# Optimization experiments

Measured on AMD Instinct MI355X. Metric: run time of the kernel, lower is better.

Reference implementation:

```python
import jax, jax.numpy as jnp
import numpy as np

HIDDEN = [256, 256, 256]
COND = 30
NB_STEPS = 20  # Clenshaw-Curtis quadrature order -> NB_STEPS+1 nodes


def cc_weights_steps(nb_steps):
    # Clenshaw-Curtis weights/nodes on [-1, 1] (UMNN compute_cc_weights)
    lam = np.arange(nb_steps + 1, dtype=np.float64).reshape(-1, 1)
    lam = np.cos(lam @ lam.T * np.pi / nb_steps)
    lam[:, 0] *= 0.5
    lam[:, -1] *= 0.5
    lam = lam * 2.0 / nb_steps
    W = np.arange(nb_steps + 1, dtype=np.float64).reshape(-1, 1)
    W[1::2] = 0.0
    W = 2.0 / (1.0 - W ** 2)
    W[0] = 1.0
    W[1::2] = 0.0
    cc_w = (lam.T @ W).flatten()          # [S]
    steps = np.cos(np.arange(nb_steps + 1) * np.pi / nb_steps)  # [S]
    return jnp.asarray(cc_w, jnp.float32), jnp.asarray(steps, jnp.float32)


def mlp(inp, Ws, bs):
    # IntegrandNet: Linear+ReLU chain, final layer ELU(x)+1 (strictly positive)
    y = inp
    n = len(Ws)
    for i in range(n):
        y = y @ Ws[i] + bs[i]
        y = jax.nn.relu(y) if i < n - 1 else jax.nn.elu(y) + 1.0
    return y[..., 0]


def setup_inputs() -> dict:
    key = jax.random.key(0)
    ks = jax.random.split(key, 12)
    B, D = 512, 32
    x = jax.random.normal(ks[0], (B, D), jnp.float32)
    h = jax.random.normal(ks[1], (B, D, COND), jnp.float32)
    dims = [1 + COND] + HIDDEN + [1]
    params = {}
    for i in range(len(dims) - 1):
        params[f"W{i}"] = jax.random.normal(ks[2 + 2 * i], (dims[i], dims[i + 1]), jnp.float32) / np.sqrt(dims[i]).astype(np.float32)
        params[f"b{i}"] = jnp.zeros((dims[i + 1],), jnp.float32)
    return {"x": x, "h": h, **params}


def reference(x, h, W0, b0, W1, b1, W2, b2, W3, b3):
    Ws = [W0, W1, W2, W3]
    bs = [b0, b1, b2, b3]
    B, D = x.shape
    S = NB_STEPS + 1
    cc_w, steps = cc_weights_steps(NB_STEPS)
    # x0 = 0, xT = x -> quadrature nodes X = xT * (steps + 1) / 2, shape [B, S, D]
    X = x[:, None, :] * (steps[None, :, None] + 1.0) * 0.5
    hb = jnp.broadcast_to(h[:, None, :, :], (B, S, D, COND))
    inp = jnp.concatenate([X[..., None], hb], axis=-1)  # [B, S, D, 1+COND]
    f = mlp(inp, Ws, bs)                                 # [B, S, D] positive integrand
    z_est = jnp.einsum('bsd,s->bd', f, cc_w) * x * 0.5   # integral over [0, x]
    z = z_est + h[:, :, 0]                               # add offset z0
    # second output: integrand evaluated at x (the transform's Jacobian diag)
    inp_x = jnp.concatenate([x[..., None], h], axis=-1)  # [B, D, 1+COND]
    jac = mlp(inp_x, Ws, bs)                             # [B, D]
    return z, jac
```

## Files before the change

### kernel.cpp

```cpp
#include <hip/hip_runtime.h>
#include <math.h>

#define NB        512
#define ND        32
#define NCOND     30
#define NS        21
#define NBD       (NB*ND)
#define NROWS     (NBD*NS)
#define MBLK      64
#define NBLOCKS   (NROWS/MBLK)

#define W0P_ELEMS (1*16*64*8)
#define W1P_ELEMS (8*16*64*8)
#define W3P_ELEMS (8*64*8)
#define WP_TOTAL  (W0P_ELEMS + 2*W1P_ELEMS + W3P_ELEMS)

typedef __bf16 bf8 __attribute__((ext_vector_type(8)));
typedef float  fx4 __attribute__((ext_vector_type(4)));
typedef unsigned short us8 __attribute__((ext_vector_type(8)));

__device__ __forceinline__ unsigned short f2bf(float f) {
  unsigned int u = __float_as_uint(f);
  u += 0x7FFFu + ((u >> 16) & 1u);
  return (unsigned short)(u >> 16);
}

__global__ void prep_pack(const float* __restrict__ W0,
                          const float* __restrict__ W1,
                          const float* __restrict__ W2,
                          const float* __restrict__ W3,
                          unsigned short* __restrict__ wp) {
  int t = blockIdx.x * blockDim.x + threadIdx.x;
  if (t >= WP_TOTAL / 8) return;
  int base = t * 8;
  us8 out;
  if (base >= W0P_ELEMS + 2 * W1P_ELEMS) {
    int rem  = base - (W0P_ELEMS + 2 * W1P_ELEMS);
    int lane = (rem >> 3) & 63;
    int ktl  = rem >> 9;
    int k0   = ktl * 32 + (lane >> 4) * 8;
#pragma unroll
    for (int i = 0; i < 8; ++i)
      out[i] = ((lane & 15) == 0) ? f2bf(W3[k0 + i]) : (unsigned short)0;
  } else {
    const float* W; int rem, K;
    if (base < W0P_ELEMS)                  { W = W0; rem = base;                 K = 31;  }
    else if (base < W0P_ELEMS + W1P_ELEMS) { W = W1; rem = base - W0P_ELEMS;     K = 256; }
    else                                   { W = W2; rem = base - W0P_ELEMS - W1P_ELEMS; K = 256; }
    int lane = (rem >> 3) & 63;
    int ct   = (rem >> 9) & 15;
    int ktl  =  rem >> 13;
    int j  = ct * 16 + (lane & 15);
    int k0 = ktl * 32 + (lane >> 4) * 8;
#pragma unroll
    for (int i = 0; i < 8; ++i) {
      int k = k0 + i;
      out[i] = (k < K) ? f2bf(W[k * 256 + j]) : (unsigned short)0;
    }
  }
  *reinterpret_cast<us8*>(wp + base) = out;
}


#define ACC_BIAS(BIAS)                                                           \
  {                                                                              \
    float4 bq0 = *reinterpret_cast<const float4*>((BIAS) + (cgrp * 4 + 0) * 16 + khalf * 4); \
    float4 bq1 = *reinterpret_cast<const float4*>((BIAS) + (cgrp * 4 + 1) * 16 + khalf * 4); \
    float4 bq2 = *reinterpret_cast<const float4*>((BIAS) + (cgrp * 4 + 2) * 16 + khalf * 4); \
    float4 bq3 = *reinterpret_cast<const float4*>((BIAS) + (cgrp * 4 + 3) * 16 + khalf * 4); \
    _Pragma("unroll")                                                            \
    for (int rt = 0; rt < 4; ++rt) {                                             \
      acc[rt][0] = fx4{bq0.x, bq0.y, bq0.z, bq0.w};                              \
      acc[rt][1] = fx4{bq1.x, bq1.y, bq1.z, bq1.w};                              \
      acc[rt][2] = fx4{bq2.x, bq2.y, bq2.z, bq2.w};                              \
      acc[rt][3] = fx4{bq3.x, bq3.y, bq3.z, bq3.w};                              \
    }                                                                            \
  }

#define LOADW4(S0,S1,S2,S3, WB, KT)                                              \
  S0 = *reinterpret_cast<const bf8*>((WB) + (((KT) * 16 + cgrp * 4 + 0) * 64 + lane) * 8); \
  S1 = *reinterpret_cast<const bf8*>((WB) + (((KT) * 16 + cgrp * 4 + 1) * 64 + lane) * 8); \
  S2 = *reinterpret_cast<const bf8*>((WB) + (((KT) * 16 + cgrp * 4 + 2) * 64 + lane) * 8); \
  S3 = *reinterpret_cast<const bf8*>((WB) + (((KT) * 16 + cgrp * 4 + 3) * 64 + lane) * 8);

#define AOFF(M, KT) (((unsigned)((M) * 512 + (KT) * 64 + khalf * 16)) ^ ((unsigned)(((M) & 15) << 4)))

#define KSTEP(SRC, W0_,W1_,W2_,W3_, KT)                                          \
  {                                                                              \
    bf8 a0 = *reinterpret_cast<const bf8*>((SRC) + AOFF( 0 + colb, KT));         \
    bf8 a1 = *reinterpret_cast<const bf8*>((SRC) + AOFF(16 + colb, KT));         \
    bf8 a2 = *reinterpret_cast<const bf8*>((SRC) + AOFF(32 + colb, KT));         \
    bf8 a3 = *reinterpret_cast<const bf8*>((SRC) + AOFF(48 + colb, KT));         \
    __builtin_amdgcn_s_setprio(1);                                               \
    acc[0][0] = __builtin_amdgcn_mfma_f32_16x16x32_bf16(W0_, a0, acc[0][0], 0, 0, 0); \
    acc[0][1] = __builtin_amdgcn_mfma_f32_16x16x32_bf16(W1_, a0, acc[0][1], 0, 0, 0); \
    acc[0][2] = __builtin_amdgcn_mfma_f32_16x16x32_bf16(W2_, a0, acc[0][2], 0, 0, 0); \
    acc[0][3] = __builtin_amdgcn_mfma_f32_16x16x32_bf16(W3_, a0, acc[0][3], 0, 0, 0); \
    acc[1][0] = __builtin_amdgcn_mfma_f32_16x16x32_bf16(W0_, a1, acc[1][0], 0, 0, 0); \
    acc[1][1] = __builtin_amdgcn_mfma_f32_16x16x32_bf16(W1_, a1, acc[1][1], 0, 0, 0); \
    acc[1][2] = __builtin_amdgcn_mfma_f32_16x16x32_bf16(W2_, a1, acc[1][2], 0, 0, 0); \
    acc[1][3] = __builtin_amdgcn_mfma_f32_16x16x32_bf16(W3_, a1, acc[1][3], 0, 0, 0); \
    acc[2][0] = __builtin_amdgcn_mfma_f32_16x16x32_bf16(W0_, a2, acc[2][0], 0, 0, 0); \
    acc[2][1] = __builtin_amdgcn_mfma_f32_16x16x32_bf16(W1_, a2, acc[2][1], 0, 0, 0); \
    acc[2][2] = __builtin_amdgcn_mfma_f32_16x16x32_bf16(W2_, a2, acc[2][2], 0, 0, 0); \
    acc[2][3] = __builtin_amdgcn_mfma_f32_16x16x32_bf16(W3_, a2, acc[2][3], 0, 0, 0); \
    acc[3][0] = __builtin_amdgcn_mfma_f32_16x16x32_bf16(W0_, a3, acc[3][0], 0, 0, 0); \
    acc[3][1] = __builtin_amdgcn_mfma_f32_16x16x32_bf16(W1_, a3, acc[3][1], 0, 0, 0); \
    acc[3][2] = __builtin_amdgcn_mfma_f32_16x16x32_bf16(W2_, a3, acc[3][2], 0, 0, 0); \
    acc[3][3] = __builtin_amdgcn_mfma_f32_16x16x32_bf16(W3_, a3, acc[3][3], 0, 0, 0); \
    __builtin_amdgcn_s_setprio(0);                                               \
  }

#define DENSE_PIPE(SRC, WB, NWB)                                                 \
  KSTEP(SRC, wa0,wa1,wa2,wa3, 0) LOADW4(wa0,wa1,wa2,wa3, WB, 2)                  \
  KSTEP(SRC, wb0,wb1,wb2,wb3, 1) LOADW4(wb0,wb1,wb2,wb3, WB, 3)                  \
  KSTEP(SRC, wa0,wa1,wa2,wa3, 2) LOADW4(wa0,wa1,wa2,wa3, WB, 4)                  \
  KSTEP(SRC, wb0,wb1,wb2,wb3, 3) LOADW4(wb0,wb1,wb2,wb3, WB, 5)                  \
  KSTEP(SRC, wa0,wa1,wa2,wa3, 4) LOADW4(wa0,wa1,wa2,wa3, WB, 6)                  \
  KSTEP(SRC, wb0,wb1,wb2,wb3, 5) LOADW4(wb0,wb1,wb2,wb3, WB, 7)                  \
  KSTEP(SRC, wa0,wa1,wa2,wa3, 6) LOADW4(wa0,wa1,wa2,wa3, NWB, 0)                 \
  KSTEP(SRC, wb0,wb1,wb2,wb3, 7) LOADW4(wb0,wb1,wb2,wb3, NWB, 1)

#define DENSE_LAST(SRC, WB)                                                      \
  KSTEP(SRC, wa0,wa1,wa2,wa3, 0) LOADW4(wa0,wa1,wa2,wa3, WB, 2)                  \
  KSTEP(SRC, wb0,wb1,wb2,wb3, 1) LOADW4(wb0,wb1,wb2,wb3, WB, 3)                  \
  KSTEP(SRC, wa0,wa1,wa2,wa3, 2) LOADW4(wa0,wa1,wa2,wa3, WB, 4)                  \
  KSTEP(SRC, wb0,wb1,wb2,wb3, 3) LOADW4(wb0,wb1,wb2,wb3, WB, 5)                  \
  KSTEP(SRC, wa0,wa1,wa2,wa3, 4) LOADW4(wa0,wa1,wa2,wa3, WB, 6)                  \
  KSTEP(SRC, wb0,wb1,wb2,wb3, 5) LOADW4(wb0,wb1,wb2,wb3, WB, 7)                  \
  KSTEP(SRC, wa0,wa1,wa2,wa3, 6)                                                 \
  KSTEP(SRC, wb0,wb1,wb2,wb3, 7)

#define ACT_STORE(DST)                                                           \
  {                                                                              \
    _Pragma("unroll")                                                            \
    for (int rt = 0; rt < 4; ++rt) {                                             \
      int m = rt * 16 + colb;                                                    \
      unsigned int sbase = (unsigned int)(m * 512);                              \
      unsigned int swz   = (unsigned int)((m & 15) << 4);                        \
      _Pragma("unroll")                                                          \
      for (int ct = 0; ct < 4; ++ct) {                                           \
        int n0 = (cgrp * 4 + ct) * 16 + khalf * 4;                               \
        float v0 = fmaxf(acc[rt][ct][0], 0.f);                                   \
        float v1 = fmaxf(acc[rt][ct][1], 0.f);                                   \
        float v2 = fmaxf(acc[rt][ct][2], 0.f);                                   \
        float v3 = fmaxf(acc[rt][ct][3], 0.f);                                   \
        unsigned int p0, p1;                                                     \
        asm("v_cvt_pk_bf16_f32 %0, %1, %2" : "=v"(p0) : "v"(v0), "v"(v1));       \
        asm("v_cvt_pk_bf16_f32 %0, %1, %2" : "=v"(p1) : "v"(v2), "v"(v3));       \
        uint2 pk; pk.x = p0; pk.y = p1;                                          \
        *reinterpret_cast<uint2*>((DST) + ((sbase + (unsigned int)(n0 * 2)) ^ swz)) = pk; \
      }                                                                          \
    }                                                                            \
  }

__global__ __launch_bounds__(256, 2)
void mlp_kernel(const float* __restrict__ x, const float* __restrict__ h,
                const float* __restrict__ b0, const float* __restrict__ b1,
                const float* __restrict__ b2, const float* __restrict__ b3,
                const unsigned short* __restrict__ wp,
                float* __restrict__ fbuf) {
  __shared__ __align__(16) unsigned char ldsA[64 * 512];
  __shared__ __align__(16) unsigned char ldsB[64 * 512];
  unsigned char* ldsIn = ldsB;

  int tid  = threadIdx.x;
  int wv   = tid >> 6;
  int lane = tid & 63;
  int cgrp = wv;
  int colb  = lane & 15;
  int khalf = lane >> 4;
  int R0 = blockIdx.x * MBLK;

  const unsigned short* wb1p = wp + W0P_ELEMS;
  const unsigned short* wb2p = wp + W0P_ELEMS + W1P_ELEMS;
  const unsigned short* w3p  = wp + W0P_ELEMS + 2 * W1P_ELEMS;

  bf8 wa0, wa1, wa2, wa3, wb0, wb1, wb2, wb3;
  LOADW4(wa0, wa1, wa2, wa3, wp, 0);

  {
    int r = tid >> 2;
    int q = tid & 3;
    int gr = R0 + r;
    unsigned int bd = (unsigned int)gr / NS;
    int s = gr - (int)bd * NS;
    float xv = x[bd];
    float node = xv * (cosf((float)s * 0.15707963267948966f) + 1.0f) * 0.5f;
    const float* hrow = h + bd * NCOND;
    us8 au;
#pragma unroll
    for (int i = 0; i < 8; ++i) {
      int c = q * 8 + i;
      float v;
      if (c == 0)       v = node;
      else if (c <= 30) v = hrow[c - 1];
      else              v = 0.0f;
      au[i] = f2bf(v);
    }
    unsigned int off = (unsigned int)(r * 64 + q * 16) ^ (unsigned int)((r & 3) << 4);
    *reinterpret_cast<us8*>(ldsIn + off) = au;
  }
  __syncthreads();

  fx4 acc[4][4];

  {
    ACC_BIAS(b0);
#pragma unroll
    for (int rt = 0; rt < 4; ++rt) {
      int m = rt * 16 + colb;
      unsigned int off = (unsigned int)(m * 64 + khalf * 16) ^ (unsigned int)((m & 3) << 4);
      bf8 a = *reinterpret_cast<const bf8*>(ldsIn + off);
      acc[rt][0] = __builtin_amdgcn_mfma_f32_16x16x32_bf16(wa0, a, acc[rt][0], 0, 0, 0);
      acc[rt][1] = __builtin_amdgcn_mfma_f32_16x16x32_bf16(wa1, a, acc[rt][1], 0, 0, 0);
      acc[rt][2] = __builtin_amdgcn_mfma_f32_16x16x32_bf16(wa2, a, acc[rt][2], 0, 0, 0);
      acc[rt][3] = __builtin_amdgcn_mfma_f32_16x16x32_bf16(wa3, a, acc[rt][3], 0, 0, 0);
    }
    LOADW4(wa0, wa1, wa2, wa3, wb1p, 0);
    LOADW4(wb0, wb1, wb2, wb3, wb1p, 1);
    ACT_STORE(ldsA);
  }
  __syncthreads();

  ACC_BIAS(b1);
  DENSE_PIPE(ldsA, wb1p, wb2p);
  ACT_STORE(ldsB);
  __syncthreads();

  ACC_BIAS(b2);
  DENSE_LAST(ldsB, wb2p);
  ACT_STORE(ldsA);
  __syncthreads();

  {
    fx4 a3 = fx4{0.f, 0.f, 0.f, 0.f};
    int m = wv * 16 + colb;
    unsigned int abase = (unsigned int)(m * 512 + khalf * 16);
    unsigned int aswz  = (unsigned int)((m & 15) << 4);
#pragma unroll
    for (int kt = 0; kt < 8; ++kt) {
      bf8 w3f = *reinterpret_cast<const bf8*>(w3p + (kt * 64 + lane) * 8);
      bf8 a = *reinterpret_cast<const bf8*>(ldsA + ((abase + (unsigned)(kt * 64)) ^ aswz));
      a3 = __builtin_amdgcn_mfma_f32_16x16x32_bf16(w3f, a, a3, 0, 0, 0);
    }
    if (lane < 16) {
      float y = a3[0] + b3[0];
      float f = (y > 0.f) ? (y + 1.f) : expf(y);
      fbuf[R0 + wv * 16 + lane] = f;
    }
  }
}

__global__ void reduce_kernel(const float* __restrict__ x, const float* __restrict__ h,
                              const float* __restrict__ fbuf, float* __restrict__ out) {
  __shared__ float ccw[NS];
  int tid = threadIdx.x;
  if (tid < NS) {
    double acc = 0.0;
#pragma unroll
    for (int i = 0; i <= 20; i += 2) {
      double wi = (i == 0) ? 1.0 : 2.0 / (1.0 - (double)(i * i));
      acc += cos((double)(i * tid) * 3.141592653589793 / 20.0) * wi;
    }
    double edge = (tid == 0 || tid == 20) ? 0.5 : 1.0;
    ccw[tid] = (float)(acc * 0.1 * edge);
  }
  __syncthreads();
  int t = blockIdx.x * blockDim.x + tid;
  if (t >= NBD) return;
  const float* fb = fbuf + t * NS;
  float acc = 0.f;
#pragma unroll
  for (int i = 0; i < NS; ++i) acc += fb[i] * ccw[i];
  float z = acc * x[t] * 0.5f + h[t * NCOND];
  out[t] = z;
  out[NBD + t] = fb[0];
}

extern "C" void kernel_launch(void* const* d_in, const int* in_sizes, int n_in,
                              void* d_out, int out_size, void* d_ws, size_t ws_size,
                              hipStream_t stream) {
  (void)in_sizes; (void)n_in; (void)out_size; (void)ws_size;
  const float* x  = (const float*)d_in[0];
  const float* h  = (const float*)d_in[1];
  const float* W0 = (const float*)d_in[2];
  const float* b0 = (const float*)d_in[3];
  const float* W1 = (const float*)d_in[4];
  const float* b1 = (const float*)d_in[5];
  const float* W2 = (const float*)d_in[6];
  const float* b2 = (const float*)d_in[7];
  const float* W3 = (const float*)d_in[8];
  const float* b3 = (const float*)d_in[9];

  unsigned short* wp = (unsigned short*)d_ws;
  float* fbuf = (float*)((char*)d_ws + WP_TOTAL * sizeof(unsigned short));
  float* out  = (float*)d_out;

  prep_pack<<<(WP_TOTAL / 8 + 255) / 256, 256, 0, stream>>>(W0, W1, W2, W3, wp);
  mlp_kernel<<<NBLOCKS, 256, 0, stream>>>(x, h, b0, b1, b2, b3, wp, fbuf);
  reduce_kernel<<<(NBD + 255) / 256, 256, 0, stream>>>(x, h, fbuf, out);
}
```

Baseline: 101.5 us.

## Split output columns across 8 waves and software-pipeline LDS activation loads

Each 64-row block now launches 512 threads (8 waves), and each wave computes 32 output columns instead of 64. This halves the per-wave accumulators and weight registers. The K loop is restructured so activation fragments for the next k-step are loaded from LDS while the current MFMAs run, with double-buffered A registers. The aim is more waves in flight to hide latency. The cost is twice the LDS activation reads per block, and only the first four waves take part in the final layer.

```diff
diff --git a/kernel.cpp b/kernel.cpp
--- a/kernel.cpp
+++ b/kernel.cpp
@@ -64,72 +64,60 @@
 
 #define ACC_BIAS(BIAS)                                                           \
   {                                                                              \
-    float4 bq0 = *reinterpret_cast<const float4*>((BIAS) + (cgrp * 4 + 0) * 16 + khalf * 4); \
-    float4 bq1 = *reinterpret_cast<const float4*>((BIAS) + (cgrp * 4 + 1) * 16 + khalf * 4); \
-    float4 bq2 = *reinterpret_cast<const float4*>((BIAS) + (cgrp * 4 + 2) * 16 + khalf * 4); \
-    float4 bq3 = *reinterpret_cast<const float4*>((BIAS) + (cgrp * 4 + 3) * 16 + khalf * 4); \
+    float4 bq0 = *reinterpret_cast<const float4*>((BIAS) + (cgrp * 2 + 0) * 16 + khalf * 4); \
+    float4 bq1 = *reinterpret_cast<const float4*>((BIAS) + (cgrp * 2 + 1) * 16 + khalf * 4); \
     _Pragma("unroll")                                                            \
     for (int rt = 0; rt < 4; ++rt) {                                             \
       acc[rt][0] = fx4{bq0.x, bq0.y, bq0.z, bq0.w};                              \
       acc[rt][1] = fx4{bq1.x, bq1.y, bq1.z, bq1.w};                              \
-      acc[rt][2] = fx4{bq2.x, bq2.y, bq2.z, bq2.w};                              \
-      acc[rt][3] = fx4{bq3.x, bq3.y, bq3.z, bq3.w};                              \
     }                                                                            \
   }
 
-#define LOADW4(S0,S1,S2,S3, WB, KT)                                              \
-  S0 = *reinterpret_cast<const bf8*>((WB) + (((KT) * 16 + cgrp * 4 + 0) * 64 + lane) * 8); \
-  S1 = *reinterpret_cast<const bf8*>((WB) + (((KT) * 16 + cgrp * 4 + 1) * 64 + lane) * 8); \
-  S2 = *reinterpret_cast<const bf8*>((WB) + (((KT) * 16 + cgrp * 4 + 2) * 64 + lane) * 8); \
-  S3 = *reinterpret_cast<const bf8*>((WB) + (((KT) * 16 + cgrp * 4 + 3) * 64 + lane) * 8);
+#define LOADW2(S0,S1, WB, KT)                                                    \
+  S0 = *reinterpret_cast<const bf8*>((WB) + (((KT) * 16 + cgrp * 2 + 0) * 64 + lane) * 8); \
+  S1 = *reinterpret_cast<const bf8*>((WB) + (((KT) * 16 + cgrp * 2 + 1) * 64 + lane) * 8);
 
 #define AOFF(M, KT) (((unsigned)((M) * 512 + (KT) * 64 + khalf * 16)) ^ ((unsigned)(((M) & 15) << 4)))
 
-#define KSTEP(SRC, W0_,W1_,W2_,W3_, KT)                                          \
-  {                                                                              \
-    bf8 a0 = *reinterpret_cast<const bf8*>((SRC) + AOFF( 0 + colb, KT));         \
-    bf8 a1 = *reinterpret_cast<const bf8*>((SRC) + AOFF(16 + colb, KT));         \
-    bf8 a2 = *reinterpret_cast<const bf8*>((SRC) + AOFF(32 + colb, KT));         \
-    bf8 a3 = *reinterpret_cast<const bf8*>((SRC) + AOFF(48 + colb, KT));         \
-    __builtin_amdgcn_s_setprio(1);                                               \
-    acc[0][0] = __builtin_amdgcn_mfma_f32_16x16x32_bf16(W0_, a0, acc[0][0], 0, 0, 0); \
-    acc[0][1] = __builtin_amdgcn_mfma_f32_16x16x32_bf16(W1_, a0, acc[0][1], 0, 0, 0); \
-    acc[0][2] = __builtin_amdgcn_mfma_f32_16x16x32_bf16(W2_, a0, acc[0][2], 0, 0, 0); \
-    acc[0][3] = __builtin_amdgcn_mfma_f32_16x16x32_bf16(W3_, a0, acc[0][3], 0, 0, 0); \
-    acc[1][0] = __builtin_amdgcn_mfma_f32_16x16x32_bf16(W0_, a1, acc[1][0], 0, 0, 0); \
-    acc[1][1] = __builtin_amdgcn_mfma_f32_16x16x32_bf16(W1_, a1, acc[1][1], 0, 0, 0); \
-    acc[1][2] = __builtin_amdgcn_mfma_f32_16x16x32_bf16(W2_, a1, acc[1][2], 0, 0, 0); \
-    acc[1][3] = __builtin_amdgcn_mfma_f32_16x16x32_bf16(W3_, a1, acc[1][3], 0, 0, 0); \
-    acc[2][0] = __builtin_amdgcn_mfma_f32_16x16x32_bf16(W0_, a2, acc[2][0], 0, 0, 0); \
-    acc[2][1] = __builtin_amdgcn_mfma_f32_16x16x32_bf16(W1_, a2, acc[2][1], 0, 0, 0); \
-    acc[2][2] = __builtin_amdgcn_mfma_f32_16x16x32_bf16(W2_, a2, acc[2][2], 0, 0, 0); \
-    acc[2][3] = __builtin_amdgcn_mfma_f32_16x16x32_bf16(W3_, a2, acc[2][3], 0, 0, 0); \
-    acc[3][0] = __builtin_amdgcn_mfma_f32_16x16x32_bf16(W0_, a3, acc[3][0], 0, 0, 0); \
-    acc[3][1] = __builtin_amdgcn_mfma_f32_16x16x32_bf16(W1_, a3, acc[3][1], 0, 0, 0); \
-    acc[3][2] = __builtin_amdgcn_mfma_f32_16x16x32_bf16(W2_, a3, acc[3][2], 0, 0, 0); \
-    acc[3][3] = __builtin_amdgcn_mfma_f32_16x16x32_bf16(W3_, a3, acc[3][3], 0, 0, 0); \
-    __builtin_amdgcn_s_setprio(0);                                               \
-  }
+#define ALOAD(A0,A1,A2,A3, SRC, KT)                                              \
+  A0 = *reinterpret_cast<const bf8*>((SRC) + AOFF( 0 + colb, KT));               \
+  A1 = *reinterpret_cast<const bf8*>((SRC) + AOFF(16 + colb, KT));               \
+  A2 = *reinterpret_cast<const bf8*>((SRC) + AOFF(32 + colb, KT));               \
+  A3 = *reinterpret_cast<const bf8*>((SRC) + AOFF(48 + colb, KT));
+
+#define KMFMA(W0_,W1_, A0,A1,A2,A3)                                              \
+  __builtin_amdgcn_s_setprio(1);                                                 \
+  acc[0][0] = __builtin_amdgcn_mfma_f32_16x16x32_bf16(W0_, A0, acc[0][0], 0, 0, 0); \
+  acc[0][1] = __builtin_amdgcn_mfma_f32_16x16x32_bf16(W1_, A0, acc[0][1], 0, 0, 0); \
+  acc[1][0] = __builtin_amdgcn_mfma_f32_16x16x32_bf16(W0_, A1, acc[1][0], 0, 0, 0); \
+  acc[1][1] = __builtin_amdgcn_mfma_f32_16x16x32_bf16(W1_, A1, acc[1][1], 0, 0, 0); \
+  acc[2][0] = __builtin_amdgcn_mfma_f32_16x16x32_bf16(W0_, A2, acc[2][0], 0, 0, 0); \
+  acc[2][1] = __builtin_amdgcn_mfma_f32_16x16x32_bf16(W1_, A2, acc[2][1], 0, 0, 0); \
+  acc[3][0] = __builtin_amdgcn_mfma_f32_16x16x32_bf16(W0_, A3, acc[3][0], 0, 0, 0); \
+  acc[3][1] = __builtin_amdgcn_mfma_f32_16x16x32_bf16(W1_, A3, acc[3][1], 0, 0, 0); \
+  __builtin_amdgcn_s_setprio(0);
 
 #define DENSE_PIPE(SRC, WB, NWB)                                                 \
-  KSTEP(SRC, wa0,wa1,wa2,wa3, 0) LOADW4(wa0,wa1,wa2,wa3, WB, 2)                  \
-  KSTEP(SRC, wb0,wb1,wb2,wb3, 1) LOADW4(wb0,wb1,wb2,wb3, WB, 3)                  \
-  KSTEP(SRC, wa0,wa1,wa2,wa3, 2) LOADW4(wa0,wa1,wa2,wa3, WB, 4)                  \
-  KSTEP(SRC, wb0,wb1,wb2,wb3, 3) LOADW4(wb0,wb1,wb2,wb3, WB, 5)                  \
-  KSTEP(SRC, wa0,wa1,wa2,wa3, 4) LOADW4(wa0,wa1,wa2,wa3, WB, 6)                  \
-  KSTEP(SRC, wb0,wb1,wb2,wb3, 5) LOADW4(wb0,wb1,wb2,wb3, WB, 7)                  \
-  KSTEP(SRC, wa0,wa1,wa2,wa3, 6) LOADW4(wa0,wa1,wa2,wa3, NWB, 0)                 \
-  KSTEP(SRC, wb0,wb1,wb2,wb3, 7) LOADW4(wb0,wb1,wb2,wb3, NWB, 1)
+  ALOAD(aa0,aa1,aa2,aa3, SRC, 0)                                                 \
+  ALOAD(ab0,ab1,ab2,ab3, SRC, 1) KMFMA(wa0,wa1, aa0,aa1,aa2,aa3) LOADW2(wa0,wa1, WB, 2) \
+  ALOAD(aa0,aa1,aa2,aa3, SRC, 2) KMFMA(wb0,wb1, ab0,ab1,ab2,ab3) LOADW2(wb0,wb1, WB, 3) \
+  ALOAD(ab0,ab1,ab2,ab3, SRC, 3) KMFMA(wa0,wa1, aa0,aa1,aa2,aa3) LOADW2(wa0,wa1, WB, 4) \
+  ALOAD(aa0,aa1,aa2,aa3, SRC, 4) KMFMA(wb0,wb1, ab0,ab1,ab2,ab3) LOADW2(wb0,wb1, WB, 5) \
+  ALOAD(ab0,ab1,ab2,ab3, SRC, 5) KMFMA(wa0,wa1, aa0,aa1,aa2,aa3) LOADW2(wa0,wa1, WB, 6) \
+  ALOAD(aa0,aa1,aa2,aa3, SRC, 6) KMFMA(wb0,wb1, ab0,ab1,ab2,ab3) LOADW2(wb0,wb1, WB, 7) \
+  ALOAD(ab0,ab1,ab2,ab3, SRC, 7) KMFMA(wa0,wa1, aa0,aa1,aa2,aa3) LOADW2(wa0,wa1, NWB, 0) \
+                                 KMFMA(wb0,wb1, ab0,ab1,ab2,ab3) LOADW2(wb0,wb1, NWB, 1)
 
 #define DENSE_LAST(SRC, WB)                                                      \
-  KSTEP(SRC, wa0,wa1,wa2,wa3, 0) LOADW4(wa0,wa1,wa2,wa3, WB, 2)                  \
-  KSTEP(SRC, wb0,wb1,wb2,wb3, 1) LOADW4(wb0,wb1,wb2,wb3, WB, 3)                  \
-  KSTEP(SRC, wa0,wa1,wa2,wa3, 2) LOADW4(wa0,wa1,wa2,wa3, WB, 4)                  \
-  KSTEP(SRC, wb0,wb1,wb2,wb3, 3) LOADW4(wb0,wb1,wb2,wb3, WB, 5)                  \
-  KSTEP(SRC, wa0,wa1,wa2,wa3, 4) LOADW4(wa0,wa1,wa2,wa3, WB, 6)                  \
-  KSTEP(SRC, wb0,wb1,wb2,wb3, 5) LOADW4(wb0,wb1,wb2,wb3, WB, 7)                  \
-  KSTEP(SRC, wa0,wa1,wa2,wa3, 6)                                                 \
-  KSTEP(SRC, wb0,wb1,wb2,wb3, 7)
+  ALOAD(aa0,aa1,aa2,aa3, SRC, 0)                                                 \
+  ALOAD(ab0,ab1,ab2,ab3, SRC, 1) KMFMA(wa0,wa1, aa0,aa1,aa2,aa3) LOADW2(wa0,wa1, WB, 2) \
+  ALOAD(aa0,aa1,aa2,aa3, SRC, 2) KMFMA(wb0,wb1, ab0,ab1,ab2,ab3) LOADW2(wb0,wb1, WB, 3) \
+  ALOAD(ab0,ab1,ab2,ab3, SRC, 3) KMFMA(wa0,wa1, aa0,aa1,aa2,aa3) LOADW2(wa0,wa1, WB, 4) \
+  ALOAD(aa0,aa1,aa2,aa3, SRC, 4) KMFMA(wb0,wb1, ab0,ab1,ab2,ab3) LOADW2(wb0,wb1, WB, 5) \
+  ALOAD(ab0,ab1,ab2,ab3, SRC, 5) KMFMA(wa0,wa1, aa0,aa1,aa2,aa3) LOADW2(wa0,wa1, WB, 6) \
+  ALOAD(aa0,aa1,aa2,aa3, SRC, 6) KMFMA(wb0,wb1, ab0,ab1,ab2,ab3) LOADW2(wb0,wb1, WB, 7) \
+  ALOAD(ab0,ab1,ab2,ab3, SRC, 7) KMFMA(wa0,wa1, aa0,aa1,aa2,aa3)                 \
+                                 KMFMA(wb0,wb1, ab0,ab1,ab2,ab3)
 
 #define ACT_STORE(DST)                                                           \
   {                                                                              \
@@ -139,8 +127,8 @@
       unsigned int sbase = (unsigned int)(m * 512);                              \
       unsigned int swz   = (unsigned int)((m & 15) << 4);                        \
       _Pragma("unroll")                                                          \
-      for (int ct = 0; ct < 4; ++ct) {                                           \
-        int n0 = (cgrp * 4 + ct) * 16 + khalf * 4;                               \
+      for (int ct = 0; ct < 2; ++ct) {                                           \
+        int n0 = (cgrp * 2 + ct) * 16 + khalf * 4;                               \
         float v0 = fmaxf(acc[rt][ct][0], 0.f);                                   \
         float v1 = fmaxf(acc[rt][ct][1], 0.f);                                   \
         float v2 = fmaxf(acc[rt][ct][2], 0.f);                                   \
@@ -154,7 +142,7 @@
     }                                                                            \
   }
 
-__global__ __launch_bounds__(256, 2)
+__global__ __launch_bounds__(512, 2)
 void mlp_kernel(const float* __restrict__ x, const float* __restrict__ h,
                 const float* __restrict__ b0, const float* __restrict__ b1,
                 const float* __restrict__ b2, const float* __restrict__ b3,
@@ -176,10 +164,11 @@
   const unsigned short* wb2p = wp + W0P_ELEMS + W1P_ELEMS;
   const unsigned short* w3p  = wp + W0P_ELEMS + 2 * W1P_ELEMS;
 
-  bf8 wa0, wa1, wa2, wa3, wb0, wb1, wb2, wb3;
-  LOADW4(wa0, wa1, wa2, wa3, wp, 0);
-
-  {
+  bf8 wa0, wa1, wb0, wb1;
+  bf8 aa0, aa1, aa2, aa3, ab0, ab1, ab2, ab3;
+  LOADW2(wa0, wa1, wp, 0);
+
+  if (tid < 256) {
     int r = tid >> 2;
     int q = tid & 3;
     int gr = R0 + r;
@@ -203,7 +192,7 @@
   }
   __syncthreads();
 
-  fx4 acc[4][4];
+  fx4 acc[4][2];
 
   {
     ACC_BIAS(b0);
@@ -214,11 +203,9 @@
       bf8 a = *reinterpret_cast<const bf8*>(ldsIn + off);
       acc[rt][0] = __builtin_amdgcn_mfma_f32_16x16x32_bf16(wa0, a, acc[rt][0], 0, 0, 0);
       acc[rt][1] = __builtin_amdgcn_mfma_f32_16x16x32_bf16(wa1, a, acc[rt][1], 0, 0, 0);
-      acc[rt][2] = __builtin_amdgcn_mfma_f32_16x16x32_bf16(wa2, a, acc[rt][2], 0, 0, 0);
-      acc[rt][3] = __builtin_amdgcn_mfma_f32_16x16x32_bf16(wa3, a, acc[rt][3], 0, 0, 0);
-    }
-    LOADW4(wa0, wa1, wa2, wa3, wb1p, 0);
-    LOADW4(wb0, wb1, wb2, wb3, wb1p, 1);
+    }
+    LOADW2(wa0, wa1, wb1p, 0);
+    LOADW2(wb0, wb1, wb1p, 1);
     ACT_STORE(ldsA);
   }
   __syncthreads();
@@ -233,7 +220,7 @@
   ACT_STORE(ldsA);
   __syncthreads();
 
-  {
+  if (wv < 4) {
     fx4 a3 = fx4{0.f, 0.f, 0.f, 0.f};
     int m = wv * 16 + colb;
     unsigned int abase = (unsigned int)(m * 512 + khalf * 16);
@@ -298,6 +285,6 @@
   float* out  = (float*)d_out;
 
   prep_pack<<<(WP_TOTAL / 8 + 255) / 256, 256, 0, stream>>>(W0, W1, W2, W3, wp);
-  mlp_kernel<<<NBLOCKS, 256, 0, stream>>>(x, h, b0, b1, b2, b3, wp, fbuf);
+  mlp_kernel<<<NBLOCKS, 512, 0, stream>>>(x, h, b0, b1, b2, b3, wp, fbuf);
   reduce_kernel<<<(NBD + 255) / 256, 256, 0, stream>>>(x, h, fbuf, out);
 }
```

Measured after the change: 110.0 us. 8.4% more time.

## Deepen weight and LDS activation prefetch pipeline in dense layers

Applied to the files above, without the earlier changes.

Replaces the two-deep weight register pipeline with a three-deep rotation (wa/wb/wc) and also double-buffers the LDS activation fragments, so the A loads for the next k-step are issued before the current MFMAs. This is meant to hide global weight-load and LDS latency behind the MFMA chain. The extra registers force launch bounds down from 2 to 1 wave-group per SIMD, which reduces occupancy and the latency hiding that came from a second resident block.

```diff
diff --git a/kernel.cpp b/kernel.cpp
--- a/kernel.cpp
+++ b/kernel.cpp
@@ -85,51 +85,31 @@
 
 #define AOFF(M, KT) (((unsigned)((M) * 512 + (KT) * 64 + khalf * 16)) ^ ((unsigned)(((M) & 15) << 4)))
 
-#define KSTEP(SRC, W0_,W1_,W2_,W3_, KT)                                          \
-  {                                                                              \
-    bf8 a0 = *reinterpret_cast<const bf8*>((SRC) + AOFF( 0 + colb, KT));         \
-    bf8 a1 = *reinterpret_cast<const bf8*>((SRC) + AOFF(16 + colb, KT));         \
-    bf8 a2 = *reinterpret_cast<const bf8*>((SRC) + AOFF(32 + colb, KT));         \
-    bf8 a3 = *reinterpret_cast<const bf8*>((SRC) + AOFF(48 + colb, KT));         \
-    __builtin_amdgcn_s_setprio(1);                                               \
-    acc[0][0] = __builtin_amdgcn_mfma_f32_16x16x32_bf16(W0_, a0, acc[0][0], 0, 0, 0); \
-    acc[0][1] = __builtin_amdgcn_mfma_f32_16x16x32_bf16(W1_, a0, acc[0][1], 0, 0, 0); \
-    acc[0][2] = __builtin_amdgcn_mfma_f32_16x16x32_bf16(W2_, a0, acc[0][2], 0, 0, 0); \
-    acc[0][3] = __builtin_amdgcn_mfma_f32_16x16x32_bf16(W3_, a0, acc[0][3], 0, 0, 0); \
-    acc[1][0] = __builtin_amdgcn_mfma_f32_16x16x32_bf16(W0_, a1, acc[1][0], 0, 0, 0); \
-    acc[1][1] = __builtin_amdgcn_mfma_f32_16x16x32_bf16(W1_, a1, acc[1][1], 0, 0, 0); \
-    acc[1][2] = __builtin_amdgcn_mfma_f32_16x16x32_bf16(W2_, a1, acc[1][2], 0, 0, 0); \
-    acc[1][3] = __builtin_amdgcn_mfma_f32_16x16x32_bf16(W3_, a1, acc[1][3], 0, 0, 0); \
-    acc[2][0] = __builtin_amdgcn_mfma_f32_16x16x32_bf16(W0_, a2, acc[2][0], 0, 0, 0); \
-    acc[2][1] = __builtin_amdgcn_mfma_f32_16x16x32_bf16(W1_, a2, acc[2][1], 0, 0, 0); \
-    acc[2][2] = __builtin_amdgcn_mfma_f32_16x16x32_bf16(W2_, a2, acc[2][2], 0, 0, 0); \
-    acc[2][3] = __builtin_amdgcn_mfma_f32_16x16x32_bf16(W3_, a2, acc[2][3], 0, 0, 0); \
-    acc[3][0] = __builtin_amdgcn_mfma_f32_16x16x32_bf16(W0_, a3, acc[3][0], 0, 0, 0); \
-    acc[3][1] = __builtin_amdgcn_mfma_f32_16x16x32_bf16(W1_, a3, acc[3][1], 0, 0, 0); \
-    acc[3][2] = __builtin_amdgcn_mfma_f32_16x16x32_bf16(W2_, a3, acc[3][2], 0, 0, 0); \
-    acc[3][3] = __builtin_amdgcn_mfma_f32_16x16x32_bf16(W3_, a3, acc[3][3], 0, 0, 0); \
-    __builtin_amdgcn_s_setprio(0);                                               \
-  }
-
-#define DENSE_PIPE(SRC, WB, NWB)                                                 \
-  KSTEP(SRC, wa0,wa1,wa2,wa3, 0) LOADW4(wa0,wa1,wa2,wa3, WB, 2)                  \
-  KSTEP(SRC, wb0,wb1,wb2,wb3, 1) LOADW4(wb0,wb1,wb2,wb3, WB, 3)                  \
-  KSTEP(SRC, wa0,wa1,wa2,wa3, 2) LOADW4(wa0,wa1,wa2,wa3, WB, 4)                  \
-  KSTEP(SRC, wb0,wb1,wb2,wb3, 3) LOADW4(wb0,wb1,wb2,wb3, WB, 5)                  \
-  KSTEP(SRC, wa0,wa1,wa2,wa3, 4) LOADW4(wa0,wa1,wa2,wa3, WB, 6)                  \
-  KSTEP(SRC, wb0,wb1,wb2,wb3, 5) LOADW4(wb0,wb1,wb2,wb3, WB, 7)                  \
-  KSTEP(SRC, wa0,wa1,wa2,wa3, 6) LOADW4(wa0,wa1,wa2,wa3, NWB, 0)                 \
-  KSTEP(SRC, wb0,wb1,wb2,wb3, 7) LOADW4(wb0,wb1,wb2,wb3, NWB, 1)
-
-#define DENSE_LAST(SRC, WB)                                                      \
-  KSTEP(SRC, wa0,wa1,wa2,wa3, 0) LOADW4(wa0,wa1,wa2,wa3, WB, 2)                  \
-  KSTEP(SRC, wb0,wb1,wb2,wb3, 1) LOADW4(wb0,wb1,wb2,wb3, WB, 3)                  \
-  KSTEP(SRC, wa0,wa1,wa2,wa3, 2) LOADW4(wa0,wa1,wa2,wa3, WB, 4)                  \
-  KSTEP(SRC, wb0,wb1,wb2,wb3, 3) LOADW4(wb0,wb1,wb2,wb3, WB, 5)                  \
-  KSTEP(SRC, wa0,wa1,wa2,wa3, 4) LOADW4(wa0,wa1,wa2,wa3, WB, 6)                  \
-  KSTEP(SRC, wb0,wb1,wb2,wb3, 5) LOADW4(wb0,wb1,wb2,wb3, WB, 7)                  \
-  KSTEP(SRC, wa0,wa1,wa2,wa3, 6)                                                 \
-  KSTEP(SRC, wb0,wb1,wb2,wb3, 7)
+#define ALOAD4(A0,A1,A2,A3, SRC, KT)                                             \
+  A0 = *reinterpret_cast<const bf8*>((SRC) + AOFF( 0 + colb, KT));               \
+  A1 = *reinterpret_cast<const bf8*>((SRC) + AOFF(16 + colb, KT));               \
+  A2 = *reinterpret_cast<const bf8*>((SRC) + AOFF(32 + colb, KT));               \
+  A3 = *reinterpret_cast<const bf8*>((SRC) + AOFF(48 + colb, KT));
+
+#define KMFMA16(W0_,W1_,W2_,W3_, A0_,A1_,A2_,A3_)                                \
+  __builtin_amdgcn_s_setprio(1);                                                 \
+  acc[0][0] = __builtin_amdgcn_mfma_f32_16x16x32_bf16(W0_, A0_, acc[0][0], 0, 0, 0); \
+  acc[0][1] = __builtin_amdgcn_mfma_f32_16x16x32_bf16(W1_, A0_, acc[0][1], 0, 0, 0); \
+  acc[0][2] = __builtin_amdgcn_mfma_f32_16x16x32_bf16(W2_, A0_, acc[0][2], 0, 0, 0); \
+  acc[0][3] = __builtin_amdgcn_mfma_f32_16x16x32_bf16(W3_, A0_, acc[0][3], 0, 0, 0); \
+  acc[1][0] = __builtin_amdgcn_mfma_f32_16x16x32_bf16(W0_, A1_, acc[1][0], 0, 0, 0); \
+  acc[1][1] = __builtin_amdgcn_mfma_f32_16x16x32_bf16(W1_, A1_, acc[1][1], 0, 0, 0); \
+  acc[1][2] = __builtin_amdgcn_mfma_f32_16x16x32_bf16(W2_, A1_, acc[1][2], 0, 0, 0); \
+  acc[1][3] = __builtin_amdgcn_mfma_f32_16x16x32_bf16(W3_, A1_, acc[1][3], 0, 0, 0); \
+  acc[2][0] = __builtin_amdgcn_mfma_f32_16x16x32_bf16(W0_, A2_, acc[2][0], 0, 0, 0); \
+  acc[2][1] = __builtin_amdgcn_mfma_f32_16x16x32_bf16(W1_, A2_, acc[2][1], 0, 0, 0); \
+  acc[2][2] = __builtin_amdgcn_mfma_f32_16x16x32_bf16(W2_, A2_, acc[2][2], 0, 0, 0); \
+  acc[2][3] = __builtin_amdgcn_mfma_f32_16x16x32_bf16(W3_, A2_, acc[2][3], 0, 0, 0); \
+  acc[3][0] = __builtin_amdgcn_mfma_f32_16x16x32_bf16(W0_, A3_, acc[3][0], 0, 0, 0); \
+  acc[3][1] = __builtin_amdgcn_mfma_f32_16x16x32_bf16(W1_, A3_, acc[3][1], 0, 0, 0); \
+  acc[3][2] = __builtin_amdgcn_mfma_f32_16x16x32_bf16(W2_, A3_, acc[3][2], 0, 0, 0); \
+  acc[3][3] = __builtin_amdgcn_mfma_f32_16x16x32_bf16(W3_, A3_, acc[3][3], 0, 0, 0); \
+  __builtin_amdgcn_s_setprio(0);
 
 #define ACT_STORE(DST)                                                           \
   {                                                                              \
@@ -154,7 +134,7 @@
     }                                                                            \
   }
 
-__global__ __launch_bounds__(256, 2)
+__global__ __launch_bounds__(256, 1)
 void mlp_kernel(const float* __restrict__ x, const float* __restrict__ h,
                 const float* __restrict__ b0, const float* __restrict__ b1,
                 const float* __restrict__ b2, const float* __restrict__ b3,
@@ -176,7 +156,8 @@
   const unsigned short* wb2p = wp + W0P_ELEMS + W1P_ELEMS;
   const unsigned short* w3p  = wp + W0P_ELEMS + 2 * W1P_ELEMS;
 
-  bf8 wa0, wa1, wa2, wa3, wb0, wb1, wb2, wb3;
+  bf8 wa0, wa1, wa2, wa3, wb0, wb1, wb2, wb3, wc0, wc1, wc2, wc3;
+  bf8 aa0, aa1, aa2, aa3, ab0, ab1, ab2, ab3;
   LOADW4(wa0, wa1, wa2, wa3, wp, 0);
 
   {
@@ -219,17 +200,36 @@
     }
     LOADW4(wa0, wa1, wa2, wa3, wb1p, 0);
     LOADW4(wb0, wb1, wb2, wb3, wb1p, 1);
+    LOADW4(wc0, wc1, wc2, wc3, wb1p, 2);
     ACT_STORE(ldsA);
   }
   __syncthreads();
 
   ACC_BIAS(b1);
-  DENSE_PIPE(ldsA, wb1p, wb2p);
+  ALOAD4(aa0,aa1,aa2,aa3, ldsA, 0);
+  ALOAD4(ab0,ab1,ab2,ab3, ldsA, 1);
+  KMFMA16(wa0,wa1,wa2,wa3, aa0,aa1,aa2,aa3); LOADW4(wa0,wa1,wa2,wa3, wb1p, 3); ALOAD4(aa0,aa1,aa2,aa3, ldsA, 2);
+  KMFMA16(wb0,wb1,wb2,wb3, ab0,ab1,ab2,ab3); LOADW4(wb0,wb1,wb2,wb3, wb1p, 4); ALOAD4(ab0,ab1,ab2,ab3, ldsA, 3);
+  KMFMA16(wc0,wc1,wc2,wc3, aa0,aa1,aa2,aa3); LOADW4(wc0,wc1,wc2,wc3, wb1p, 5); ALOAD4(aa0,aa1,aa2,aa3, ldsA, 4);
+  KMFMA16(wa0,wa1,wa2,wa3, ab0,ab1,ab2,ab3); LOADW4(wa0,wa1,wa2,wa3, wb1p, 6); ALOAD4(ab0,ab1,ab2,ab3, ldsA, 5);
+  KMFMA16(wb0,wb1,wb2,wb3, aa0,aa1,aa2,aa3); LOADW4(wb0,wb1,wb2,wb3, wb1p, 7); ALOAD4(aa0,aa1,aa2,aa3, ldsA, 6);
+  KMFMA16(wc0,wc1,wc2,wc3, ab0,ab1,ab2,ab3); LOADW4(wc0,wc1,wc2,wc3, wb2p, 0); ALOAD4(ab0,ab1,ab2,ab3, ldsA, 7);
+  KMFMA16(wa0,wa1,wa2,wa3, aa0,aa1,aa2,aa3); LOADW4(wa0,wa1,wa2,wa3, wb2p, 1);
+  KMFMA16(wb0,wb1,wb2,wb3, ab0,ab1,ab2,ab3); LOADW4(wb0,wb1,wb2,wb3, wb2p, 2);
   ACT_STORE(ldsB);
   __syncthreads();
 
   ACC_BIAS(b2);
-  DENSE_LAST(ldsB, wb2p);
+  ALOAD4(aa0,aa1,aa2,aa3, ldsB, 0);
+  ALOAD4(ab0,ab1,ab2,ab3, ldsB, 1);
+  KMFMA16(wc0,wc1,wc2,wc3, aa0,aa1,aa2,aa3); LOADW4(wc0,wc1,wc2,wc3, wb2p, 3); ALOAD4(aa0,aa1,aa2,aa3, ldsB, 2);
+  KMFMA16(wa0,wa1,wa2,wa3, ab0,ab1,ab2,ab3); LOADW4(wa0,wa1,wa2,wa3, wb2p, 4); ALOAD4(ab0,ab1,ab2,ab3, ldsB, 3);
+  KMFMA16(wb0,wb1,wb2,wb3, aa0,aa1,aa2,aa3); LOADW4(wb0,wb1,wb2,wb3, wb2p, 5); ALOAD4(aa0,aa1,aa2,aa3, ldsB, 4);
+  KMFMA16(wc0,wc1,wc2,wc3, ab0,ab1,ab2,ab3); LOADW4(wc0,wc1,wc2,wc3, wb2p, 6); ALOAD4(ab0,ab1,ab2,ab3, ldsB, 5);
+  KMFMA16(wa0,wa1,wa2,wa3, aa0,aa1,aa2,aa3); LOADW4(wa0,wa1,wa2,wa3, wb2p, 7); ALOAD4(aa0,aa1,aa2,aa3, ldsB, 6);
+  KMFMA16(wb0,wb1,wb2,wb3, ab0,ab1,ab2,ab3); ALOAD4(ab0,ab1,ab2,ab3, ldsB, 7);
+  KMFMA16(wc0,wc1,wc2,wc3, aa0,aa1,aa2,aa3);
+  KMFMA16(wa0,wa1,wa2,wa3, ab0,ab1,ab2,ab3);
   ACT_STORE(ldsA);
   __syncthreads();
 
```

After: 103.1 us. About the same (+1.6%).

## Fuse quadrature reduction into MLP kernel by aligning blocks to whole (b,d) pairs

Applied to the files above, without the earlier changes.

Blocks now process 3 complete (b,d) pairs (63 rows plus one padding row), so the 21-node quadrature sum and jac output can be computed in-block from shared memory. This removes the separate reduce kernel launch and the global fbuf round trip. The Clenshaw-Curtis weights are computed once in the prep kernel. In exchange about 1/64 of the MFMA work is wasted on padding rows and the block count rises slightly.

```diff
diff --git a/kernel.cpp b/kernel.cpp
--- a/kernel.cpp
+++ b/kernel.cpp
@@ -6,9 +6,8 @@
 #define NCOND     30
 #define NS        21
 #define NBD       (NB*ND)
-#define NROWS     (NBD*NS)
-#define MBLK      64
-#define NBLOCKS   (NROWS/MBLK)
+#define BDPB      3
+#define NBLK      ((NBD + BDPB - 1) / BDPB)
 
 #define W0P_ELEMS (1*16*64*8)
 #define W1P_ELEMS (8*16*64*8)
@@ -29,7 +28,19 @@
                           const float* __restrict__ W1,
                           const float* __restrict__ W2,
                           const float* __restrict__ W3,
-                          unsigned short* __restrict__ wp) {
+                          unsigned short* __restrict__ wp,
+                          float* __restrict__ ccwbuf) {
+  if (blockIdx.x == 0 && threadIdx.x < NS) {
+    int tid = threadIdx.x;
+    double acc = 0.0;
+#pragma unroll
+    for (int i = 0; i <= 20; i += 2) {
+      double wi = (i == 0) ? 1.0 : 2.0 / (1.0 - (double)(i * i));
+      acc += cos((double)(i * tid) * 3.141592653589793 / 20.0) * wi;
+    }
+    double edge = (tid == 0 || tid == 20) ? 0.5 : 1.0;
+    ccwbuf[tid] = (float)(acc * 0.1 * edge);
+  }
   int t = blockIdx.x * blockDim.x + threadIdx.x;
   if (t >= WP_TOTAL / 8) return;
   int base = t * 8;
@@ -159,9 +170,11 @@
                 const float* __restrict__ b0, const float* __restrict__ b1,
                 const float* __restrict__ b2, const float* __restrict__ b3,
                 const unsigned short* __restrict__ wp,
-                float* __restrict__ fbuf) {
+                const float* __restrict__ ccw,
+                float* __restrict__ out) {
   __shared__ __align__(16) unsigned char ldsA[64 * 512];
   __shared__ __align__(16) unsigned char ldsB[64 * 512];
+  __shared__ float ldsF[64];
   unsigned char* ldsIn = ldsB;
 
   int tid  = threadIdx.x;
@@ -170,7 +183,7 @@
   int cgrp = wv;
   int colb  = lane & 15;
   int khalf = lane >> 4;
-  int R0 = blockIdx.x * MBLK;
+  int blkbd = blockIdx.x * BDPB;
 
   const unsigned short* wb1p = wp + W0P_ELEMS;
   const unsigned short* wb2p = wp + W0P_ELEMS + W1P_ELEMS;
@@ -182,21 +195,23 @@
   {
     int r = tid >> 2;
     int q = tid & 3;
-    int gr = R0 + r;
-    unsigned int bd = (unsigned int)gr / NS;
-    int s = gr - (int)bd * NS;
-    float xv = x[bd];
-    float node = xv * (cosf((float)s * 0.15707963267948966f) + 1.0f) * 0.5f;
-    const float* hrow = h + bd * NCOND;
-    us8 au;
-#pragma unroll
-    for (int i = 0; i < 8; ++i) {
-      int c = q * 8 + i;
-      float v;
-      if (c == 0)       v = node;
-      else if (c <= 30) v = hrow[c - 1];
-      else              v = 0.0f;
-      au[i] = f2bf(v);
+    unsigned int u = (unsigned int)r / NS;
+    int s = r - (int)u * NS;
+    int bd = blkbd + (int)u;
+    us8 au = us8{0,0,0,0,0,0,0,0};
+    if (r < 63 && bd < NBD) {
+      float xv = x[bd];
+      float node = xv * (cosf((float)s * 0.15707963267948966f) + 1.0f) * 0.5f;
+      const float* hrow = h + bd * NCOND;
+#pragma unroll
+      for (int i = 0; i < 8; ++i) {
+        int c = q * 8 + i;
+        float v;
+        if (c == 0)       v = node;
+        else if (c <= 30) v = hrow[c - 1];
+        else              v = 0.0f;
+        au[i] = f2bf(v);
+      }
     }
     unsigned int off = (unsigned int)(r * 64 + q * 16) ^ (unsigned int)((r & 3) << 4);
     *reinterpret_cast<us8*>(ldsIn + off) = au;
@@ -247,35 +262,21 @@
     if (lane < 16) {
       float y = a3[0] + b3[0];
       float f = (y > 0.f) ? (y + 1.f) : expf(y);
-      fbuf[R0 + wv * 16 + lane] = f;
-    }
-  }
-}
-
-__global__ void reduce_kernel(const float* __restrict__ x, const float* __restrict__ h,
-                              const float* __restrict__ fbuf, float* __restrict__ out) {
-  __shared__ float ccw[NS];
-  int tid = threadIdx.x;
-  if (tid < NS) {
-    double acc = 0.0;
-#pragma unroll
-    for (int i = 0; i <= 20; i += 2) {
-      double wi = (i == 0) ? 1.0 : 2.0 / (1.0 - (double)(i * i));
-      acc += cos((double)(i * tid) * 3.141592653589793 / 20.0) * wi;
-    }
-    double edge = (tid == 0 || tid == 20) ? 0.5 : 1.0;
-    ccw[tid] = (float)(acc * 0.1 * edge);
-  }
-  __syncthreads();
-  int t = blockIdx.x * blockDim.x + tid;
-  if (t >= NBD) return;
-  const float* fb = fbuf + t * NS;
-  float acc = 0.f;
-#pragma unroll
-  for (int i = 0; i < NS; ++i) acc += fb[i] * ccw[i];
-  float z = acc * x[t] * 0.5f + h[t * NCOND];
-  out[t] = z;
-  out[NBD + t] = fb[0];
+      ldsF[wv * 16 + lane] = f;
+    }
+  }
+  __syncthreads();
+
+  if (tid < BDPB) {
+    int bd = blkbd + tid;
+    if (bd < NBD) {
+      float acc2 = 0.f;
+#pragma unroll
+      for (int s2 = 0; s2 < NS; ++s2) acc2 += ldsF[tid * NS + s2] * ccw[s2];
+      out[bd] = acc2 * x[bd] * 0.5f + h[bd * NCOND];
+      out[NBD + bd] = ldsF[tid * NS];
+    }
+  }
 }
 
 extern "C" void kernel_launch(void* const* d_in, const int* in_sizes, int n_in,
@@ -294,10 +295,9 @@
   const float* b3 = (const float*)d_in[9];
 
   unsigned short* wp = (unsigned short*)d_ws;
-  float* fbuf = (float*)((char*)d_ws + WP_TOTAL * sizeof(unsigned short));
+  float* ccwbuf = (float*)((char*)d_ws + WP_TOTAL * sizeof(unsigned short));
   float* out  = (float*)d_out;
 
-  prep_pack<<<(WP_TOTAL / 8 + 255) / 256, 256, 0, stream>>>(W0, W1, W2, W3, wp);
-  mlp_kernel<<<NBLOCKS, 256, 0, stream>>>(x, h, b0, b1, b2, b3, wp, fbuf);
-  reduce_kernel<<<(NBD + 255) / 256, 256, 0, stream>>>(x, h, fbuf, out);
+  prep_pack<<<(WP_TOTAL / 8 + 255) / 256, 256, 0, stream>>>(W0, W1, W2, W3, wp, ccwbuf);
+  mlp_kernel<<<NBLK, 256, 0, stream>>>(x, h, b0, b1, b2, b3, wp, ccwbuf, out);
 }
```

After: 101.0 us, median of 2. Within noise of the previous version (-0.4%).
